# Optimization experiments

Hardware: AMD Instinct MI355X
Metric: run time of the kernel (lower is better)

The kernel has to match this reference:

```python
import jax, jax.numpy as jnp
import numpy as np

B, S, D, H = 4, 2048, 256, 8
SPARSITY = 0.1


def setup_inputs() -> dict:
    key = jax.random.key(0)
    ks = jax.random.split(key, 6)
    s = 0.02
    return {
        "x": jax.random.normal(ks[0], (B, S, D), jnp.float32),
        # nn.MultiheadAttention packed in-projection (W_q;W_k;W_v) and out-projection
        "w_in": jax.random.normal(ks[1], (3 * D, D), jnp.float32) * s,
        "b_in": jnp.zeros((3 * D,), jnp.float32),
        "w_out": jax.random.normal(ks[2], (D, D), jnp.float32) * s,
        "b_out": jnp.zeros((D,), jnp.float32),
        # sparsity gate: Linear(D, D//4) -> ReLU -> Linear(D//4, 1) -> Sigmoid
        "gate_w1": jax.random.normal(ks[3], (D // 4, D), jnp.float32) * s,
        "gate_b1": jnp.zeros((D // 4,), jnp.float32),
        "gate_w2": jax.random.normal(ks[4], (1, D // 4), jnp.float32) * s,
        "gate_b2": jnp.zeros((1,), jnp.float32),
    }


def reference(x, w_in, b_in, w_out, b_out, gate_w1, gate_b1, gate_w2, gate_b2):
    b, s, d = x.shape
    hd = d // H

    # --- adaptive sparse mask (top-k importance gating) ---
    h = jax.nn.relu(jnp.einsum('bsd,fd->bsf', x, gate_w1) + gate_b1)
    importance = jax.nn.sigmoid(jnp.einsum('bsf,of->bso', h, gate_w2) + gate_b2)[..., 0]  # [B,S]
    k = max(1, int(s * SPARSITY))
    _, top_idx = jax.lax.top_k(importance, k)  # [B,k]
    keep = jnp.zeros((b, s), dtype=bool).at[jnp.arange(b)[:, None], top_idx].set(True)  # [B,S]

    # --- multi-head attention with key_padding_mask = ~keep ---
    qkv = jnp.einsum('bsd,ed->bse', x, w_in) + b_in  # [B,S,3D]
    q, kk, v = jnp.split(qkv, 3, axis=-1)
    split_heads = lambda t: t.reshape(b, s, H, hd).transpose(0, 2, 1, 3)  # [B,H,S,hd]
    q, kk, v = split_heads(q), split_heads(kk), split_heads(v)

    scores = jnp.einsum('bhqd,bhkd->bhqk', q, kk) / jnp.sqrt(jnp.asarray(hd, x.dtype))
    neg = jnp.finfo(scores.dtype).min
    scores = jnp.where(keep[:, None, None, :], scores, neg)  # mask non-selected keys
    attn = jax.nn.softmax(scores, axis=-1)

    out = jnp.einsum('bhqk,bhkd->bhqd', attn, v)
    out = out.transpose(0, 2, 1, 3).reshape(b, s, d)
    return jnp.einsum('bsd,od->bso', out, w_out) + b_out
```

## Files before the change

kernel.cpp:

```cpp
#include <hip/hip_runtime.h>
#include <hip/hip_bf16.h>

#define B_  4
#define S_  2048
#define D_  256
#define H_  8
#define HD_ 32
#define K_  204
#define SCALE_ 0.17677669529663687f

#define OFF_IMP    0
#define OFF_META   8192
#define OFF_KIDX   8208
#define OFF_KV     9232
#define OFF_Q      218128
#define OFF_XH     1266704
#define OFF_XL     2315280
#define OFF_AOH    3363856
#define OFF_AOL    4412432
#define OFF_WIH    5461008
#define OFF_WIL    5559312
#define OFF_WOH    5657616
#define OFF_WOL    5690384

#define GSTR 80
#define PSTR 228
#define VSTR 228

typedef __attribute__((ext_vector_type(8))) short short8v;
typedef __attribute__((ext_vector_type(4))) float f32x4;

static __device__ __forceinline__ unsigned short f2bf(float f) {
    unsigned int u = __float_as_uint(f);
    u += 0x7FFFu + ((u >> 16) & 1u);
    return (unsigned short)(u >> 16);
}
static __device__ __forceinline__ float bf2f(unsigned short h) {
    return __uint_as_float((unsigned int)h << 16);
}
static __device__ __forceinline__ short8v ld_bf8(const unsigned short* p) {
    union { unsigned int u[4]; short8v v; } cv;
    const uint2 a  = *(const uint2*)(p);
    const uint2 b2 = *(const uint2*)(p + 4);
    cv.u[0] = a.x; cv.u[1] = a.y; cv.u[2] = b2.x; cv.u[3] = b2.y;
    return cv.v;
}
static __device__ __forceinline__ void split_store8(
    const float* __restrict__ src, unsigned short* dh, unsigned short* dl)
{
    short8v h, l;
    #pragma unroll
    for (int e = 0; e < 8; ++e) {
        const float f = src[e];
        const unsigned short hh = f2bf(f);
        h[e] = (short)hh;
        l[e] = (short)f2bf(f - bf2f(hh));
    }
    *(short8v*)dh = h;
    *(short8v*)dl = l;
}

__global__ __launch_bounds__(256) void gate_kernel(
    const float* __restrict__ x, const float* __restrict__ gw1,
    const float* __restrict__ gb1, const float* __restrict__ gw2,
    const float* __restrict__ w_in, const float* __restrict__ w_out, float* ws)
{
    const int t0 = blockIdx.x * 8;
    const int tid = threadIdx.x;
    __shared__ __align__(16) float xs[8 * D_];
    __shared__ float hred[8 * 64];

    const float4* src = (const float4*)(x + (size_t)t0 * D_);
    ((float4*)xs)[tid]       = src[tid];
    ((float4*)xs)[tid + 256] = src[tid + 256];
    __syncthreads();

    {
        unsigned short* XH = (unsigned short*)(ws + OFF_XH);
        unsigned short* XL = (unsigned short*)(ws + OFF_XL);
        split_store8(xs + tid * 8, XH + (size_t)t0 * D_ + tid * 8,
                                   XL + (size_t)t0 * D_ + tid * 8);
    }
    if (blockIdx.x < 128) {
        const int e0 = blockIdx.x * 2048 + tid * 8;
        if (e0 < 196608) {
            split_store8(w_in + e0, (unsigned short*)(ws + OFF_WIH) + e0,
                                    (unsigned short*)(ws + OFF_WIL) + e0);
        } else {
            const int e = e0 - 196608;
            split_store8(w_out + e, (unsigned short*)(ws + OFF_WOH) + e,
                                    (unsigned short*)(ws + OFF_WOL) + e);
        }
    }
    if (blockIdx.x == 0 && tid < 16) ((int*)(ws + OFF_META))[tid] = 0;

    const int c = tid & 3, f = tid >> 2;
    float4 wv[16];
    const float4* wr = (const float4*)(gw1 + (size_t)f * D_) + c;
    #pragma unroll
    for (int j = 0; j < 16; ++j) wv[j] = wr[j * 4];
    const float bb = gb1[f], g2 = gw2[f];

    #pragma unroll
    for (int tk = 0; tk < 8; ++tk) {
        const float4* xr = (const float4*)(xs + tk * D_) + c;
        float a = 0.0f;
        #pragma unroll
        for (int j = 0; j < 16; ++j) {
            float4 xv = xr[j * 4];
            a += wv[j].x*xv.x + wv[j].y*xv.y + wv[j].z*xv.z + wv[j].w*xv.w;
        }
        a += __shfl_xor(a, 1);
        a += __shfl_xor(a, 2);
        if (c == 0) hred[tk * 64 + f] = fmaxf(a + bb, 0.0f) * g2;
    }
    __syncthreads();

    const int tk = tid >> 5, ln = tid & 31;
    float s = hred[tk * 64 + ln] + hred[tk * 64 + ln + 32];
    #pragma unroll
    for (int o = 16; o; o >>= 1) s += __shfl_xor(s, o, 32);
    if (ln == 0) ws[OFF_IMP + t0 + tk] = s;
}

__global__ __launch_bounds__(256) void rank_kernel(
    const float* __restrict__ ws_imp, int* kidx, int* meta)
{
    const int b  = blockIdx.x >> 7;
    const int ic = blockIdx.x & 127;
    const int tid = threadIdx.x;
    __shared__ __align__(16) float vs[S_];
    const float* src = ws_imp + b * S_;
    #pragma unroll
    for (int cc = 0; cc < 2; ++cc)
        ((float4*)vs)[tid + cc*256] = ((const float4*)src)[tid + cc*256];
    __syncthreads();

    const int il = tid >> 4;
    const int c  = tid & 15;
    const int i  = ic * 16 + il;
    const float vi = vs[i];
    int gt = 0, eq = 0;
    const float4* v4 = (const float4*)vs + c * 32;
    #pragma unroll 8
    for (int t = 0; t < 32; ++t) {
        const int j4 = (t + c) & 31;
        float4 w = v4[j4];
        const int base = c * 128 + j4 * 4;
        gt += (w.x > vi); eq += (w.x == vi) && (base + 0 < i);
        gt += (w.y > vi); eq += (w.y == vi) && (base + 1 < i);
        gt += (w.z > vi); eq += (w.z == vi) && (base + 2 < i);
        gt += (w.w > vi); eq += (w.w == vi) && (base + 3 < i);
    }
    int r = gt + eq;
    r += __shfl_xor(r, 1);
    r += __shfl_xor(r, 2);
    r += __shfl_xor(r, 4);
    r += __shfl_xor(r, 8);
    if (c == 0 && r < K_) {
        const int p = atomicAdd(&meta[2 + b], 1);
        kidx[b * K_ + p] = i;
    }
}

__global__ __launch_bounds__(256) void kvg_kernel(
    const unsigned short* __restrict__ XH, const unsigned short* __restrict__ XL,
    const unsigned short* __restrict__ WKH, const unsigned short* __restrict__ WKL,
    const float* __restrict__ b_in, unsigned short* __restrict__ KV,
    const int* __restrict__ kidx)
{
    __shared__ __align__(16) unsigned short Ash[64 * GSTR];
    __shared__ __align__(16) unsigned short Asl[64 * GSTR];
    __shared__ __align__(16) unsigned short Bsh[64 * GSTR];
    __shared__ __align__(16) unsigned short Bsl[64 * GSTR];

    const int tid = threadIdx.x;
    const int b = blockIdx.y;
    const int m0 = (blockIdx.x & 3) * 64, n0 = (blockIdx.x >> 2) * 64;
    const int lane = tid & 63, w = tid >> 6;
    const int c = lane & 15, g = lane >> 4;
    const int mq = w >> 1, nq = w & 1;

    const f32x4 zf = {0.0f, 0.0f, 0.0f, 0.0f};
    f32x4 acc[2][2] = {{zf, zf}, {zf, zf}};

    const int srow = tid >> 2, sseg = tid & 3;
    const int tok = kidx[b * K_ + min(m0 + srow, K_ - 1)];
    const unsigned short* Aph = XH + ((size_t)b * S_ + tok) * D_ + sseg * 16;
    const unsigned short* Apl = XL + ((size_t)b * S_ + tok) * D_ + sseg * 16;
    const unsigned short* Bph = WKH + (size_t)(n0 + srow) * D_ + sseg * 16;
    const unsigned short* Bpl = WKL + (size_t)(n0 + srow) * D_ + sseg * 16;

    short8v arh[2], arl[2], brh[2], brl[2];
    #pragma unroll
    for (int u = 0; u < 2; ++u) {
        arh[u] = *(const short8v*)(Aph + u*8); arl[u] = *(const short8v*)(Apl + u*8);
        brh[u] = *(const short8v*)(Bph + u*8); brl[u] = *(const short8v*)(Bpl + u*8);
    }

    for (int k0 = 0; k0 < D_; k0 += 64) {
        __syncthreads();
        #pragma unroll
        for (int u = 0; u < 2; ++u) {
            *(short8v*)&Ash[srow*GSTR + sseg*16 + u*8] = arh[u];
            *(short8v*)&Asl[srow*GSTR + sseg*16 + u*8] = arl[u];
            *(short8v*)&Bsh[srow*GSTR + sseg*16 + u*8] = brh[u];
            *(short8v*)&Bsl[srow*GSTR + sseg*16 + u*8] = brl[u];
        }
        __syncthreads();
        if (k0 + 64 < D_) {
            #pragma unroll
            for (int u = 0; u < 2; ++u) {
                arh[u] = *(const short8v*)(Aph + k0 + 64 + u*8);
                arl[u] = *(const short8v*)(Apl + k0 + 64 + u*8);
                brh[u] = *(const short8v*)(Bph + k0 + 64 + u*8);
                brl[u] = *(const short8v*)(Bpl + k0 + 64 + u*8);
            }
        }
        #pragma unroll
        for (int ks = 0; ks < 2; ++ks) {
            short8v am[2][2], bm[2][2];
            #pragma unroll
            for (int t = 0; t < 2; ++t) {
                const int ra = (mq*32 + t*16 + c) * GSTR + ks*32 + g*8;
                am[t][0] = *(const short8v*)&Ash[ra];
                am[t][1] = *(const short8v*)&Asl[ra];
                const int rb = (nq*32 + t*16 + c) * GSTR + ks*32 + g*8;
                bm[t][0] = *(const short8v*)&Bsh[rb];
                bm[t][1] = *(const short8v*)&Bsl[rb];
            }
            #pragma unroll
            for (int mt = 0; mt < 2; ++mt)
                #pragma unroll
                for (int nt = 0; nt < 2; ++nt) {
                    acc[mt][nt] = __builtin_amdgcn_mfma_f32_16x16x32_bf16(am[mt][0], bm[nt][0], acc[mt][nt], 0, 0, 0);
                    acc[mt][nt] = __builtin_amdgcn_mfma_f32_16x16x32_bf16(am[mt][0], bm[nt][1], acc[mt][nt], 0, 0, 0);
                    acc[mt][nt] = __builtin_amdgcn_mfma_f32_16x16x32_bf16(am[mt][1], bm[nt][0], acc[mt][nt], 0, 0, 0);
                }
        }
    }
    #pragma unroll
    for (int nt = 0; nt < 2; ++nt) {
        const int n = n0 + nq*32 + nt*16 + c;
        const float bv = b_in[D_ + n];
        #pragma unroll
        for (int mt = 0; mt < 2; ++mt) {
            const int j = m0 + mq*32 + mt*16 + g*4;
            #pragma unroll
            for (int r = 0; r < 4; ++r)
                if (j + r < K_)
                    KV[((size_t)b * K_ + j + r) * 512 + n] = f2bf(acc[mt][nt][r] + bv);
        }
    }
}

template<bool QOUT>
__global__ __launch_bounds__(256) void gemm_kernel(
    const unsigned short* __restrict__ Ah, const unsigned short* __restrict__ Al,
    const unsigned short* __restrict__ Bh, const unsigned short* __restrict__ Bl,
    const float* __restrict__ bias, float* __restrict__ Cf,
    unsigned short* __restrict__ Cq)
{
    __shared__ __align__(16) unsigned short Ash[64 * GSTR];
    __shared__ __align__(16) unsigned short Asl[64 * GSTR];
    __shared__ __align__(16) unsigned short Bsh[64 * GSTR];
    __shared__ __align__(16) unsigned short Bsl[64 * GSTR];

    const int tid = threadIdx.x;
    const int m0 = blockIdx.x * 64, n0 = blockIdx.y * 64;
    const int lane = tid & 63, w = tid >> 6;
    const int c = lane & 15, g = lane >> 4;
    const int mq = w >> 1, nq = w & 1;

    const f32x4 zf = {0.0f, 0.0f, 0.0f, 0.0f};
    f32x4 acc[2][2] = {{zf, zf}, {zf, zf}};

    const int srow = tid >> 2, sseg = tid & 3;
    const unsigned short* Aph = Ah + (size_t)(m0 + srow) * D_ + sseg * 16;
    const unsigned short* Apl = Al + (size_t)(m0 + srow) * D_ + sseg * 16;
    const unsigned short* Bph = Bh + (size_t)(n0 + srow) * D_ + sseg * 16;
    const unsigned short* Bpl = Bl + (size_t)(n0 + srow) * D_ + sseg * 16;

    short8v arh[2], arl[2], brh[2], brl[2];
    #pragma unroll
    for (int u = 0; u < 2; ++u) {
        arh[u] = *(const short8v*)(Aph + u*8); arl[u] = *(const short8v*)(Apl + u*8);
        brh[u] = *(const short8v*)(Bph + u*8); brl[u] = *(const short8v*)(Bpl + u*8);
    }

    for (int k0 = 0; k0 < D_; k0 += 64) {
        __syncthreads();
        #pragma unroll
        for (int u = 0; u < 2; ++u) {
            *(short8v*)&Ash[srow*GSTR + sseg*16 + u*8] = arh[u];
            *(short8v*)&Asl[srow*GSTR + sseg*16 + u*8] = arl[u];
            *(short8v*)&Bsh[srow*GSTR + sseg*16 + u*8] = brh[u];
            *(short8v*)&Bsl[srow*GSTR + sseg*16 + u*8] = brl[u];
        }
        __syncthreads();
        if (k0 + 64 < D_) {
            #pragma unroll
            for (int u = 0; u < 2; ++u) {
                arh[u] = *(const short8v*)(Aph + k0 + 64 + u*8);
                arl[u] = *(const short8v*)(Apl + k0 + 64 + u*8);
                brh[u] = *(const short8v*)(Bph + k0 + 64 + u*8);
                brl[u] = *(const short8v*)(Bpl + k0 + 64 + u*8);
            }
        }
        #pragma unroll
        for (int ks = 0; ks < 2; ++ks) {
            short8v am[2][2], bm[2][2];
            #pragma unroll
            for (int t = 0; t < 2; ++t) {
                const int ra = (mq*32 + t*16 + c) * GSTR + ks*32 + g*8;
                am[t][0] = *(const short8v*)&Ash[ra];
                am[t][1] = *(const short8v*)&Asl[ra];
                const int rb = (nq*32 + t*16 + c) * GSTR + ks*32 + g*8;
                bm[t][0] = *(const short8v*)&Bsh[rb];
                bm[t][1] = *(const short8v*)&Bsl[rb];
            }
            #pragma unroll
            for (int mt = 0; mt < 2; ++mt)
                #pragma unroll
                for (int nt = 0; nt < 2; ++nt) {
                    acc[mt][nt] = __builtin_amdgcn_mfma_f32_16x16x32_bf16(am[mt][0], bm[nt][0], acc[mt][nt], 0, 0, 0);
                    acc[mt][nt] = __builtin_amdgcn_mfma_f32_16x16x32_bf16(am[mt][0], bm[nt][1], acc[mt][nt], 0, 0, 0);
                    acc[mt][nt] = __builtin_amdgcn_mfma_f32_16x16x32_bf16(am[mt][1], bm[nt][0], acc[mt][nt], 0, 0, 0);
                }
        }
    }
    #pragma unroll
    for (int nt = 0; nt < 2; ++nt) {
        const int n = n0 + nq*32 + nt*16 + c;
        const float bv = bias[n];
        #pragma unroll
        for (int mt = 0; mt < 2; ++mt) {
            const int m = m0 + mq*32 + mt*16 + g*4;
            #pragma unroll
            for (int r = 0; r < 4; ++r) {
                const float v = acc[mt][nt][r] + bv;
                if (QOUT) Cq[(size_t)(m + r) * D_ + n] = f2bf(v);
                else      Cf[(size_t)(m + r) * D_ + n] = v;
            }
        }
    }
}

__global__ __launch_bounds__(256) void attn_kernel(
    const unsigned short* __restrict__ KV, const unsigned short* __restrict__ Qb,
    unsigned short* __restrict__ aoh, unsigned short* __restrict__ aol)
{
    const int b = blockIdx.z, h = blockIdx.y, q0 = blockIdx.x * 32;
    const int tid = threadIdx.x;
    const int lane = tid & 63, w = tid >> 6;
    const int c = lane & 15, g = lane >> 4;

    __shared__ __align__(16) unsigned short Pl[32 * PSTR];
    __shared__ __align__(16) unsigned short VTl[32 * VSTR];
    __shared__ float redl[4 * 32];
    __shared__ float invl[32];

    const unsigned short* KVb = KV + (size_t)b * K_ * 512;

    for (int i = tid; i < K_ * 4; i += 256) {
        const int j = i >> 2, dc = i & 3;
        const short8v v = *(const short8v*)(KVb + (size_t)j * 512 + 256 + h * HD_ + dc * 8);
        #pragma unroll
        for (int r = 0; r < 8; ++r)
            VTl[(dc*8 + r)*VSTR + j] = (unsigned short)v[r];
    }
    {
        const int q = tid >> 3, cc = tid & 7;
        *(unsigned int*)&Pl[q * PSTR + 208 + cc * 2] = 0u;
    }
    for (int i = tid; i < 32 * 20; i += 256) {
        VTl[(i / 20) * VSTR + 204 + (i % 20)] = 0;
    }

    short8v qa[2];
    #pragma unroll
    for (int qt = 0; qt < 2; ++qt)
        qa[qt] = *(const short8v*)(Qb + (size_t)(b * S_ + q0 + qt*16 + c) * D_ + h * HD_ + g * 8);

    const int njt = (w == 0) ? 4 : 3;
    f32x4 acc[2][4];
    const f32x4 zf = {0.0f, 0.0f, 0.0f, 0.0f};
    #pragma unroll
    for (int qt = 0; qt < 2; ++qt)
        #pragma unroll
        for (int t = 0; t < 4; ++t) acc[qt][t] = zf;

    for (int t = 0; t < njt; ++t) {
        const int jt = w + 4 * t;
        const int jc = min(jt * 16 + c, K_ - 1);
        const short8v kb = *(const short8v*)(KVb + (size_t)jc * 512 + h * HD_ + g * 8);
        acc[0][t] = __builtin_amdgcn_mfma_f32_16x16x32_bf16(qa[0], kb, acc[0][t], 0, 0, 0);
        acc[1][t] = __builtin_amdgcn_mfma_f32_16x16x32_bf16(qa[1], kb, acc[1][t], 0, 0, 0);
    }

    float rs[2][4] = {{0,0,0,0},{0,0,0,0}};
    for (int t = 0; t < njt; ++t) {
        const int jg = (w + 4 * t) * 16 + c;
        const bool val = (jg < K_);
        #pragma unroll
        for (int qt = 0; qt < 2; ++qt) {
            #pragma unroll
            for (int r = 0; r < 4; ++r) {
                const float e = val ? __expf(acc[qt][t][r] * SCALE_) : 0.0f;
                rs[qt][r] += e;
                Pl[(qt*16 + g*4 + r) * PSTR + jg] = f2bf(e);
            }
        }
    }
    #pragma unroll
    for (int qt = 0; qt < 2; ++qt)
        #pragma unroll
        for (int r = 0; r < 4; ++r) {
            float s = rs[qt][r];
            s += __shfl_xor(s, 1); s += __shfl_xor(s, 2);
            s += __shfl_xor(s, 4); s += __shfl_xor(s, 8);
            if (c == 0) redl[w * 32 + qt*16 + g*4 + r] = s;
        }

    __syncthreads();
    if (tid < 32)
        invl[tid] = 1.0f / (redl[tid] + redl[32 + tid] + redl[64 + tid] + redl[96 + tid]);
    __syncthreads();

    const int dt = w >> 1, qt2 = w & 1;
    f32x4 o = zf;
    const unsigned short* vb = &VTl[(dt*16 + c) * VSTR];
    const unsigned short* pb = &Pl[(qt2*16 + c) * PSTR];
    #pragma unroll
    for (int kt = 0; kt < 7; ++kt) {
        const short8v av = ld_bf8(vb + kt*32 + g*8);
        const short8v bv = ld_bf8(pb + kt*32 + g*8);
        o = __builtin_amdgcn_mfma_f32_16x16x32_bf16(av, bv, o, 0, 0, 0);
    }
    const float iv = invl[qt2*16 + c];
    const size_t oidx = (size_t)(b * S_ + q0 + qt2*16 + c) * D_ + h * HD_ + dt*16 + g*4;
    ushort4 hh, ll;
    {
        const float v0 = o[0]*iv, v1 = o[1]*iv, v2 = o[2]*iv, v3 = o[3]*iv;
        hh.x = f2bf(v0); ll.x = f2bf(v0 - bf2f(hh.x));
        hh.y = f2bf(v1); ll.y = f2bf(v1 - bf2f(hh.y));
        hh.z = f2bf(v2); ll.z = f2bf(v2 - bf2f(hh.z));
        hh.w = f2bf(v3); ll.w = f2bf(v3 - bf2f(hh.w));
    }
    *(ushort4*)(aoh + oidx) = hh;
    *(ushort4*)(aol + oidx) = ll;
}

extern "C" void kernel_launch(void* const* d_in, const int* in_sizes, int n_in,
                              void* d_out, int out_size, void* d_ws, size_t ws_size,
                              hipStream_t stream)
{
    const float* x     = (const float*)d_in[0];
    const float* w_in  = (const float*)d_in[1];
    const float* b_in  = (const float*)d_in[2];
    const float* w_out = (const float*)d_in[3];
    const float* b_out = (const float*)d_in[4];
    const float* gw1   = (const float*)d_in[5];
    const float* gb1   = (const float*)d_in[6];
    const float* gw2   = (const float*)d_in[7];

    float* ws = (float*)d_ws;
    int* meta = (int*)(ws + OFF_META);
    int* kidx = (int*)(ws + OFF_KIDX);
    unsigned short* KV  = (unsigned short*)(ws + OFF_KV);
    unsigned short* Qb  = (unsigned short*)(ws + OFF_Q);
    unsigned short* XH  = (unsigned short*)(ws + OFF_XH);
    unsigned short* XL  = (unsigned short*)(ws + OFF_XL);
    unsigned short* AOH = (unsigned short*)(ws + OFF_AOH);
    unsigned short* AOL = (unsigned short*)(ws + OFF_AOL);
    unsigned short* WIH = (unsigned short*)(ws + OFF_WIH);
    unsigned short* WIL = (unsigned short*)(ws + OFF_WIL);
    unsigned short* WOH = (unsigned short*)(ws + OFF_WOH);
    unsigned short* WOL = (unsigned short*)(ws + OFF_WOL);
    float* out = (float*)d_out;

    gate_kernel<<<B_ * S_ / 8, 256, 0, stream>>>(x, gw1, gb1, gw2, w_in, w_out, ws);
    rank_kernel<<<B_ * 128, 256, 0, stream>>>(ws + OFF_IMP, kidx, meta);
    kvg_kernel<<<dim3(32, B_), 256, 0, stream>>>(
        XH, XL, WIH + 65536, WIL + 65536, b_in, KV, kidx);
    gemm_kernel<true><<<dim3(B_ * S_ / 64, D_ / 64), 256, 0, stream>>>(
        XH, XL, WIH, WIL, b_in, nullptr, Qb);
    attn_kernel<<<dim3(S_ / 32, H_, B_), 256, 0, stream>>>(KV, Qb, AOH, AOL);
    gemm_kernel<false><<<dim3(B_ * S_ / 64, D_ / 64), 256, 0, stream>>>(
        AOH, AOL, WOH, WOL, b_out, out, nullptr);
}
```

Baseline: 146.1 us.

## Merge Q and K/V projections into one launch and pre-transpose V globally

Combines the gathered K/V projection and the full Q projection into a single kernel, using blockIdx.x to pick the role, which removes one launch and lets the two run side by side. K and V are now stored separately: K row-major with stride 256, and V already transposed and zero-padded to 224 columns. The attention kernel can then load V into shared memory with vectorized copies instead of a per-element scalar transpose in every block. In exchange, the projection writes V with strided scalar stores, and the V shared-memory stride changes.

```diff
diff --git a/kernel.cpp b/kernel.cpp
--- a/kernel.cpp
+++ b/kernel.cpp
@@ -12,20 +12,21 @@
 #define OFF_IMP    0
 #define OFF_META   8192
 #define OFF_KIDX   8208
-#define OFF_KV     9232
-#define OFF_Q      218128
-#define OFF_XH     1266704
-#define OFF_XL     2315280
-#define OFF_AOH    3363856
-#define OFF_AOL    4412432
-#define OFF_WIH    5461008
-#define OFF_WIL    5559312
-#define OFF_WOH    5657616
-#define OFF_WOL    5690384
+#define OFF_KG     9232
+#define OFF_VT     113680
+#define OFF_Q      228368
+#define OFF_XH     1276944
+#define OFF_XL     2325520
+#define OFF_AOH    3374096
+#define OFF_AOL    4422672
+#define OFF_WIH    5471248
+#define OFF_WIL    5569552
+#define OFF_WOH    5667856
+#define OFF_WOL    5700624
 
 #define GSTR 80
 #define PSTR 228
-#define VSTR 228
+#define VSTR 232
 
 typedef __attribute__((ext_vector_type(8))) short short8v;
 typedef __attribute__((ext_vector_type(4))) float f32x4;
@@ -163,10 +164,11 @@
     }
 }
 
-__global__ __launch_bounds__(256) void kvg_kernel(
+__global__ __launch_bounds__(256) void proj_kernel(
     const unsigned short* __restrict__ XH, const unsigned short* __restrict__ XL,
-    const unsigned short* __restrict__ WKH, const unsigned short* __restrict__ WKL,
-    const float* __restrict__ b_in, unsigned short* __restrict__ KV,
+    const unsigned short* __restrict__ WIH, const unsigned short* __restrict__ WIL,
+    const float* __restrict__ b_in, unsigned short* __restrict__ Qb,
+    unsigned short* __restrict__ KG, unsigned short* __restrict__ VTg,
     const int* __restrict__ kidx)
 {
     __shared__ __align__(16) unsigned short Ash[64 * GSTR];
@@ -175,21 +177,33 @@
     __shared__ __align__(16) unsigned short Bsl[64 * GSTR];
 
     const int tid = threadIdx.x;
-    const int b = blockIdx.y;
-    const int m0 = (blockIdx.x & 3) * 64, n0 = (blockIdx.x >> 2) * 64;
+    const bool isQ = (blockIdx.x < 128);
     const int lane = tid & 63, w = tid >> 6;
     const int c = lane & 15, g = lane >> 4;
     const int mq = w >> 1, nq = w & 1;
+    const int srow = tid >> 2, sseg = tid & 3;
+
+    int m0, n0, b = blockIdx.y;
+    size_t arow;
+    int brow;
+    if (isQ) {
+        m0 = blockIdx.x * 64; n0 = blockIdx.y * 64;
+        arow = (size_t)(m0 + srow);
+        brow = n0 + srow;
+    } else {
+        const int kx = blockIdx.x - 128;
+        m0 = (kx & 3) * 64; n0 = (kx >> 2) * 64;
+        const int tok = kidx[b * K_ + min(m0 + srow, K_ - 1)];
+        arow = (size_t)b * S_ + tok;
+        brow = D_ + n0 + srow;
+    }
+    const unsigned short* Aph = XH + arow * D_ + sseg * 16;
+    const unsigned short* Apl = XL + arow * D_ + sseg * 16;
+    const unsigned short* Bph = WIH + (size_t)brow * D_ + sseg * 16;
+    const unsigned short* Bpl = WIL + (size_t)brow * D_ + sseg * 16;
 
     const f32x4 zf = {0.0f, 0.0f, 0.0f, 0.0f};
     f32x4 acc[2][2] = {{zf, zf}, {zf, zf}};
-
-    const int srow = tid >> 2, sseg = tid & 3;
-    const int tok = kidx[b * K_ + min(m0 + srow, K_ - 1)];
-    const unsigned short* Aph = XH + ((size_t)b * S_ + tok) * D_ + sseg * 16;
-    const unsigned short* Apl = XL + ((size_t)b * S_ + tok) * D_ + sseg * 16;
-    const unsigned short* Bph = WKH + (size_t)(n0 + srow) * D_ + sseg * 16;
-    const unsigned short* Bpl = WKL + (size_t)(n0 + srow) * D_ + sseg * 16;
 
     short8v arh[2], arl[2], brh[2], brl[2];
     #pragma unroll
@@ -239,27 +253,49 @@
                 }
         }
     }
-    #pragma unroll
-    for (int nt = 0; nt < 2; ++nt) {
-        const int n = n0 + nq*32 + nt*16 + c;
-        const float bv = b_in[D_ + n];
-        #pragma unroll
-        for (int mt = 0; mt < 2; ++mt) {
-            const int j = m0 + mq*32 + mt*16 + g*4;
-            #pragma unroll
-            for (int r = 0; r < 4; ++r)
-                if (j + r < K_)
-                    KV[((size_t)b * K_ + j + r) * 512 + n] = f2bf(acc[mt][nt][r] + bv);
-        }
-    }
-}
-
-template<bool QOUT>
+
+    if (isQ) {
+        #pragma unroll
+        for (int nt = 0; nt < 2; ++nt) {
+            const int n = n0 + nq*32 + nt*16 + c;
+            const float bv = b_in[n];
+            #pragma unroll
+            for (int mt = 0; mt < 2; ++mt) {
+                const int m = m0 + mq*32 + mt*16 + g*4;
+                #pragma unroll
+                for (int r = 0; r < 4; ++r)
+                    Qb[(size_t)(m + r) * D_ + n] = f2bf(acc[mt][nt][r] + bv);
+            }
+        }
+    } else {
+        #pragma unroll
+        for (int nt = 0; nt < 2; ++nt) {
+            const int n = n0 + nq*32 + nt*16 + c;
+            const float bv = b_in[D_ + n];
+            #pragma unroll
+            for (int mt = 0; mt < 2; ++mt) {
+                const int j = m0 + mq*32 + mt*16 + g*4;
+                #pragma unroll
+                for (int r = 0; r < 4; ++r) {
+                    const int jj = j + r;
+                    if (n < 256) {
+                        if (jj < K_)
+                            KG[((size_t)b * K_ + jj) * 256 + n] = f2bf(acc[mt][nt][r] + bv);
+                    } else {
+                        if (jj < 224)
+                            VTg[((size_t)b * 256 + (n - 256)) * 224 + jj] =
+                                (jj < K_) ? f2bf(acc[mt][nt][r] + bv) : (unsigned short)0;
+                    }
+                }
+            }
+        }
+    }
+}
+
 __global__ __launch_bounds__(256) void gemm_kernel(
     const unsigned short* __restrict__ Ah, const unsigned short* __restrict__ Al,
     const unsigned short* __restrict__ Bh, const unsigned short* __restrict__ Bl,
-    const float* __restrict__ bias, float* __restrict__ Cf,
-    unsigned short* __restrict__ Cq)
+    const float* __restrict__ bias, float* __restrict__ Cf)
 {
     __shared__ __align__(16) unsigned short Ash[64 * GSTR];
     __shared__ __align__(16) unsigned short Asl[64 * GSTR];
@@ -337,17 +373,15 @@
         for (int mt = 0; mt < 2; ++mt) {
             const int m = m0 + mq*32 + mt*16 + g*4;
             #pragma unroll
-            for (int r = 0; r < 4; ++r) {
-                const float v = acc[mt][nt][r] + bv;
-                if (QOUT) Cq[(size_t)(m + r) * D_ + n] = f2bf(v);
-                else      Cf[(size_t)(m + r) * D_ + n] = v;
-            }
+            for (int r = 0; r < 4; ++r)
+                Cf[(size_t)(m + r) * D_ + n] = acc[mt][nt][r] + bv;
         }
     }
 }
 
 __global__ __launch_bounds__(256) void attn_kernel(
-    const unsigned short* __restrict__ KV, const unsigned short* __restrict__ Qb,
+    const unsigned short* __restrict__ KG, const unsigned short* __restrict__ VTg,
+    const unsigned short* __restrict__ Qb,
     unsigned short* __restrict__ aoh, unsigned short* __restrict__ aol)
 {
     const int b = blockIdx.z, h = blockIdx.y, q0 = blockIdx.x * 32;
@@ -360,22 +394,19 @@
     __shared__ float redl[4 * 32];
     __shared__ float invl[32];
 
-    const unsigned short* KVb = KV + (size_t)b * K_ * 512;
-
-    for (int i = tid; i < K_ * 4; i += 256) {
-        const int j = i >> 2, dc = i & 3;
-        const short8v v = *(const short8v*)(KVb + (size_t)j * 512 + 256 + h * HD_ + dc * 8);
-        #pragma unroll
-        for (int r = 0; r < 8; ++r)
-            VTl[(dc*8 + r)*VSTR + j] = (unsigned short)v[r];
+    const unsigned short* KGb = KG + (size_t)b * K_ * 256;
+
+    {
+        const unsigned short* vsrc = VTg + ((size_t)b * 256 + h * HD_) * 224;
+        for (int i = tid; i < 32 * 28; i += 256) {
+            const int d = i / 28, seg = i % 28;
+            *(short8v*)&VTl[d * VSTR + seg * 8] = *(const short8v*)(vsrc + d * 224 + seg * 8);
+        }
     }
     {
         const int q = tid >> 3, cc = tid & 7;
         *(unsigned int*)&Pl[q * PSTR + 208 + cc * 2] = 0u;
     }
-    for (int i = tid; i < 32 * 20; i += 256) {
-        VTl[(i / 20) * VSTR + 204 + (i % 20)] = 0;
-    }
 
     short8v qa[2];
     #pragma unroll
@@ -393,7 +424,7 @@
     for (int t = 0; t < njt; ++t) {
         const int jt = w + 4 * t;
         const int jc = min(jt * 16 + c, K_ - 1);
-        const short8v kb = *(const short8v*)(KVb + (size_t)jc * 512 + h * HD_ + g * 8);
+        const short8v kb = *(const short8v*)(KGb + (size_t)jc * 256 + h * HD_ + g * 8);
         acc[0][t] = __builtin_amdgcn_mfma_f32_16x16x32_bf16(qa[0], kb, acc[0][t], 0, 0, 0);
         acc[1][t] = __builtin_amdgcn_mfma_f32_16x16x32_bf16(qa[1], kb, acc[1][t], 0, 0, 0);
     }
@@ -467,7 +498,8 @@
     float* ws = (float*)d_ws;
     int* meta = (int*)(ws + OFF_META);
     int* kidx = (int*)(ws + OFF_KIDX);
-    unsigned short* KV  = (unsigned short*)(ws + OFF_KV);
+    unsigned short* KG  = (unsigned short*)(ws + OFF_KG);
+    unsigned short* VTg = (unsigned short*)(ws + OFF_VT);
     unsigned short* Qb  = (unsigned short*)(ws + OFF_Q);
     unsigned short* XH  = (unsigned short*)(ws + OFF_XH);
     unsigned short* XL  = (unsigned short*)(ws + OFF_XL);
@@ -481,11 +513,9 @@
 
     gate_kernel<<<B_ * S_ / 8, 256, 0, stream>>>(x, gw1, gb1, gw2, w_in, w_out, ws);
     rank_kernel<<<B_ * 128, 256, 0, stream>>>(ws + OFF_IMP, kidx, meta);
-    kvg_kernel<<<dim3(32, B_), 256, 0, stream>>>(
-        XH, XL, WIH + 65536, WIL + 65536, b_in, KV, kidx);
-    gemm_kernel<true><<<dim3(B_ * S_ / 64, D_ / 64), 256, 0, stream>>>(
-        XH, XL, WIH, WIL, b_in, nullptr, Qb);
-    attn_kernel<<<dim3(S_ / 32, H_, B_), 256, 0, stream>>>(KV, Qb, AOH, AOL);
-    gemm_kernel<false><<<dim3(B_ * S_ / 64, D_ / 64), 256, 0, stream>>>(
-        AOH, AOL, WOH, WOL, b_out, out, nullptr);
-}
+    proj_kernel<<<dim3(160, 4), 256, 0, stream>>>(
+        XH, XL, WIH, WIL, b_in, Qb, KG, VTg, kidx);
+    attn_kernel<<<dim3(S_ / 32, H_, B_), 256, 0, stream>>>(KG, VTg, Qb, AOH, AOL);
+    gemm_kernel<<<dim3(B_ * S_ / 64, D_ / 64), 256, 0, stream>>>(
+        AOH, AOL, WOH, WOL, b_out, out);
+}
```

After: 143.5 us (median of 2 runs). No clear change (-1.8%).
